# Performance work log

Hardware: AMD Instinct MI355X
Metric: run time of the kernel (lower is better)

Reference implementation:

```python
import jax, jax.numpy as jnp
import numpy as np

WINDOW_SIZE = 3
SIGMA = 1.5
C1 = 0.01 ** 2
C2 = 0.03 ** 2


def gaussian_window(channel, window_size=WINDOW_SIZE, sigma=SIGMA):
    x = jnp.arange(window_size, dtype=jnp.float32) - window_size // 2
    g1 = jnp.exp(-(x ** 2) / (2.0 * sigma ** 2))
    g1 = g1 / g1.sum()
    g2 = jnp.outer(g1, g1)  # [k, k]
    # depthwise kernel OIHW: [C, 1, k, k]
    return jnp.broadcast_to(g2, (channel, 1, window_size, window_size))


def depthwise_conv(x, window, channel, window_size=WINDOW_SIZE):
    pad = window_size // 2
    return jax.lax.conv_general_dilated(
        x, window,
        window_strides=(1, 1),
        padding=((pad, pad), (pad, pad)),
        dimension_numbers=('NCHW', 'OIHW', 'NCHW'),
        feature_group_count=channel,
    )


def setup_inputs() -> dict:
    key = jax.random.key(0)
    k1, k2 = jax.random.split(key)
    img1 = jax.random.uniform(k1, (32, 3, 512, 512), dtype=jnp.float32)
    img2 = jax.random.uniform(k2, (32, 3, 512, 512), dtype=jnp.float32)
    return {"img1": img1, "img2": img2}


def reference(img1, img2):
    channel = img1.shape[1]
    window = gaussian_window(channel)

    mu1 = depthwise_conv(img1, window, channel)
    mu2 = depthwise_conv(img2, window, channel)
    mu1_sq = mu1 * mu1
    mu2_sq = mu2 * mu2
    mu1_mu2 = mu1 * mu2

    sigma1_sq = depthwise_conv(img1 * img1, window, channel) - mu1_sq
    sigma2_sq = depthwise_conv(img2 * img2, window, channel) - mu2_sq
    sigma12 = depthwise_conv(img1 * img2, window, channel) - mu1_mu2

    ssim_map = ((2.0 * mu1_mu2 + C1) * (2.0 * sigma12 + C2)) / (
        (mu1_sq + mu2_sq + C1) * (sigma1_sq + sigma2_sq + C2))

    # size_sum defaults to True inside ssim() -> scalar sum
    return 1.0 - ssim_map.sum()
```

## Files before the change

kernel.cpp:

```cpp
#include <hip/hip_runtime.h>

#define IMG_H 512
#define IMG_W 512
#define RH 32


__global__ __launch_bounds__(256) void ssim_main_kernel(
    const float* __restrict__ img1, const float* __restrict__ img2,
    double* __restrict__ partial)
{
    constexpr float W_E = 0.30780133f;
    constexpr float W_C = 0.38439734f;
    constexpr float C1c = 1e-4f;
    constexpr float C2c = 9e-4f;

    const int t = threadIdx.x;
    const int y0 = blockIdx.x * RH;
    const size_t base = (size_t)blockIdx.y * (size_t)(IMG_H * IMG_W);
    const float* __restrict__ A = img1 + base;
    const float* __restrict__ B = img2 + base;
    const bool has_l = (t > 0);
    const bool has_r = (t < 255);
    const int x = 2 * t;

    float h1[2][3], h2[2][3], h11[2][3], h22[2][3], h12[2][3];

    float tsum = 0.0f;

    float a00, a01, a02, a03, b00, b01, b02, b03;
    float a10, a11, a12, a13, b10, b11, b12, b13;

#define LOADROW(AP, BP, OFF) do {                                   \
    const float2 _ma = *(const float2*)(A + (OFF));                 \
    const float2 _mb = *(const float2*)(B + (OFF));                 \
    AP##1 = _ma.x; AP##2 = _ma.y; BP##1 = _mb.x; BP##2 = _mb.y;     \
    AP##0 = has_l ? A[(OFF) - 1] : 0.0f;                            \
    AP##3 = has_r ? A[(OFF) + 2] : 0.0f;                            \
    BP##0 = has_l ? B[(OFF) - 1] : 0.0f;                            \
    BP##3 = has_r ? B[(OFF) + 2] : 0.0f;                            \
} while (0)

#define ZEROROW(AP, BP) do {                                        \
    AP##0 = 0.f; AP##1 = 0.f; AP##2 = 0.f; AP##3 = 0.f;             \
    BP##0 = 0.f; BP##1 = 0.f; BP##2 = 0.f; BP##3 = 0.f;             \
} while (0)

#define HPASS(AP, BP, S) do {                                               \
    const float sa0 = AP##0 * AP##0, sa1 = AP##1 * AP##1;                   \
    const float sa2 = AP##2 * AP##2, sa3 = AP##3 * AP##3;                   \
    const float sb0 = BP##0 * BP##0, sb1 = BP##1 * BP##1;                   \
    const float sb2 = BP##2 * BP##2, sb3 = BP##3 * BP##3;                   \
    const float p0 = AP##0 * BP##0, p1 = AP##1 * BP##1;                     \
    const float p2 = AP##2 * BP##2, p3 = AP##3 * BP##3;                     \
    h1[0][S]  = W_E * (AP##0 + AP##2) + W_C * AP##1;                        \
    h1[1][S]  = W_E * (AP##1 + AP##3) + W_C * AP##2;                        \
    h2[0][S]  = W_E * (BP##0 + BP##2) + W_C * BP##1;                        \
    h2[1][S]  = W_E * (BP##1 + BP##3) + W_C * BP##2;                        \
    h11[0][S] = W_E * (sa0 + sa2) + W_C * sa1;                              \
    h11[1][S] = W_E * (sa1 + sa3) + W_C * sa2;                              \
    h22[0][S] = W_E * (sb0 + sb2) + W_C * sb1;                              \
    h22[1][S] = W_E * (sb1 + sb3) + W_C * sb2;                              \
    h12[0][S] = W_E * (p0 + p2) + W_C * p1;                                 \
    h12[1][S] = W_E * (p1 + p3) + W_C * p2;                                 \
} while (0)

#define VOUT(E0, E1, MID) do {                                              \
    _Pragma("unroll")                                                       \
    for (int c = 0; c < 2; ++c) {                                           \
        const float mu1 = W_E * (h1[c][E0] + h1[c][E1]) + W_C * h1[c][MID]; \
        const float mu2 = W_E * (h2[c][E0] + h2[c][E1]) + W_C * h2[c][MID]; \
        const float e11 = W_E * (h11[c][E0] + h11[c][E1]) + W_C * h11[c][MID]; \
        const float e22 = W_E * (h22[c][E0] + h22[c][E1]) + W_C * h22[c][MID]; \
        const float e12 = W_E * (h12[c][E0] + h12[c][E1]) + W_C * h12[c][MID]; \
        const float mu1s = mu1 * mu1, mu2s = mu2 * mu2, m12 = mu1 * mu2;    \
        const float s11 = e11 - mu1s, s22 = e22 - mu2s, s12 = e12 - m12;    \
        const float num = (2.0f * m12 + C1c) * (2.0f * s12 + C2c);          \
        const float den = (mu1s + mu2s + C1c) * (s11 + s22 + C2c);          \
        tsum += num / den;                                                  \
    }                                                                       \
} while (0)

    size_t off = (size_t)y0 * IMG_W + x;

    if (blockIdx.x != 0) LOADROW(a0, b0, off - IMG_W); else ZEROROW(a0, b0);
    LOADROW(a1, b1, off);
    HPASS(a0, b0, 0);
    LOADROW(a0, b0, off + IMG_W);
    HPASS(a1, b1, 1);
    off += 2 * (size_t)IMG_W;

#pragma unroll 1
    for (int g = 0; g < 5; ++g) {
        LOADROW(a1, b1, off); off += IMG_W; HPASS(a0, b0, 2); VOUT(2, 0, 1);
        LOADROW(a0, b0, off); off += IMG_W; HPASS(a1, b1, 0); VOUT(0, 1, 2);
        LOADROW(a1, b1, off); off += IMG_W; HPASS(a0, b0, 1); VOUT(1, 2, 0);
        LOADROW(a0, b0, off); off += IMG_W; HPASS(a1, b1, 2); VOUT(2, 0, 1);
        LOADROW(a1, b1, off); off += IMG_W; HPASS(a0, b0, 0); VOUT(0, 1, 2);
        LOADROW(a0, b0, off); off += IMG_W; HPASS(a1, b1, 1); VOUT(1, 2, 0);
    }

    if (blockIdx.x != (IMG_H / RH - 1)) LOADROW(a1, b1, off); else ZEROROW(a1, b1);
    HPASS(a0, b0, 2); VOUT(2, 0, 1);
    HPASS(a1, b1, 0); VOUT(0, 1, 2);

#undef LOADROW
#undef ZEROROW
#undef HPASS
#undef VOUT

#pragma unroll
    for (int o = 32; o >= 1; o >>= 1)
        tsum += __shfl_xor(tsum, o, 64);

    __shared__ float wpart[4];
    if ((t & 63) == 0) wpart[t >> 6] = tsum;
    __syncthreads();
    if (t == 0) {
        partial[(size_t)blockIdx.y * gridDim.x + blockIdx.x] =
            (double)wpart[0] + (double)wpart[1] +
            (double)wpart[2] + (double)wpart[3];
    }
}

__global__ __launch_bounds__(256) void ssim_fin_kernel(
    const double* __restrict__ partial, float* __restrict__ out, int n)
{
    const int t = threadIdx.x;
    double s = 0.0;
    for (int i = t; i < n; i += 256) s += partial[i];
#pragma unroll
    for (int o = 32; o >= 1; o >>= 1)
        s += __shfl_xor(s, o, 64);
    __shared__ double w[4];
    if ((t & 63) == 0) w[t >> 6] = s;
    __syncthreads();
    if (t == 0)
        out[0] = 1.0f - (float)(w[0] + w[1] + w[2] + w[3]);
}

extern "C" void kernel_launch(void* const* d_in, const int* in_sizes, int n_in,
                              void* d_out, int out_size, void* d_ws, size_t ws_size,
                              hipStream_t stream) {
    const float* img1 = (const float*)d_in[0];
    const float* img2 = (const float*)d_in[1];
    float* out = (float*)d_out;
    double* partial = (double*)d_ws;

    const int planes = in_sizes[0] / (IMG_H * IMG_W);
    const int nblk = IMG_H / RH;

    dim3 grid(nblk, planes);
    ssim_main_kernel<<<grid, 256, 0, stream>>>(img1, img2, partial);
    ssim_fin_kernel<<<1, 256, 0, stream>>>(partial, out, nblk * planes);
}
```

Measured before the change: 227.7 us.

## Stage rows in double-buffered LDS and prefetch three rows ahead

```diff
diff --git a/kernel.cpp b/kernel.cpp
--- a/kernel.cpp
+++ b/kernel.cpp
@@ -3,7 +3,10 @@
 #define IMG_H 512
 #define IMG_W 512
 #define RH 32
+#define NBX (IMG_H / RH)
 
+
+typedef float v2f __attribute__((ext_vector_type(2), aligned(8)));
 
 __global__ __launch_bounds__(256) void ssim_main_kernel(
     const float* __restrict__ img1, const float* __restrict__ img2,
@@ -19,93 +22,127 @@
     const size_t base = (size_t)blockIdx.y * (size_t)(IMG_H * IMG_W);
     const float* __restrict__ A = img1 + base;
     const float* __restrict__ B = img2 + base;
-    const bool has_l = (t > 0);
-    const bool has_r = (t < 255);
     const int x = 2 * t;
 
+    __shared__ float lsA[2][3][520];
+    __shared__ float lsB[2][3][520];
+    if (t < 24) {
+        const int col = (t & 1) * 513;
+        const int q = t >> 1;
+        const int r = q % 3;
+        const int bu = (q / 3) & 1;
+        if (q < 6) lsA[bu][r][col] = 0.0f;
+        else       lsB[bu][r][col] = 0.0f;
+    }
+
+    v2f zz; zz.x = 0.0f; zz.y = 0.0f;
+
+    v2f sa0, sa1, sa2, sb0, sb1, sb2;
+
     float h1[2][3], h2[2][3], h11[2][3], h22[2][3], h12[2][3];
-
     float tsum = 0.0f;
 
-    float a00, a01, a02, a03, b00, b01, b02, b03;
-    float a10, a11, a12, a13, b10, b11, b12, b13;
-
-#define LOADROW(AP, BP, OFF) do {                                   \
-    const float2 _ma = *(const float2*)(A + (OFF));                 \
-    const float2 _mb = *(const float2*)(B + (OFF));                 \
-    AP##1 = _ma.x; AP##2 = _ma.y; BP##1 = _mb.x; BP##2 = _mb.y;     \
-    AP##0 = has_l ? A[(OFF) - 1] : 0.0f;                            \
-    AP##3 = has_r ? A[(OFF) + 2] : 0.0f;                            \
-    BP##0 = has_l ? B[(OFF) - 1] : 0.0f;                            \
-    BP##3 = has_r ? B[(OFF) + 2] : 0.0f;                            \
+#define LOAD3(SROW) do {                                                      \
+    const int g_ = (SROW);                                                    \
+    sa0 = (g_ >= 0 && g_ < IMG_H) ? *(const v2f*)(A + (size_t)g_ * IMG_W + x) : zz;       \
+    sb0 = (g_ >= 0 && g_ < IMG_H) ? *(const v2f*)(B + (size_t)g_ * IMG_W + x) : zz;       \
+    sa1 = (g_ + 1 < IMG_H) ? *(const v2f*)(A + (size_t)(g_ + 1) * IMG_W + x) : zz;        \
+    sb1 = (g_ + 1 < IMG_H) ? *(const v2f*)(B + (size_t)(g_ + 1) * IMG_W + x) : zz;        \
+    sa2 = (g_ + 2 < IMG_H) ? *(const v2f*)(A + (size_t)(g_ + 2) * IMG_W + x) : zz;        \
+    sb2 = (g_ + 2 < IMG_H) ? *(const v2f*)(B + (size_t)(g_ + 2) * IMG_W + x) : zz;        \
 } while (0)
 
-#define ZEROROW(AP, BP) do {                                        \
-    AP##0 = 0.f; AP##1 = 0.f; AP##2 = 0.f; AP##3 = 0.f;             \
-    BP##0 = 0.f; BP##1 = 0.f; BP##2 = 0.f; BP##3 = 0.f;             \
+#define WRITE3(BU) do {                                                       \
+    lsA[BU][0][1 + x] = sa0.x; lsA[BU][0][2 + x] = sa0.y;                     \
+    lsA[BU][1][1 + x] = sa1.x; lsA[BU][1][2 + x] = sa1.y;                     \
+    lsA[BU][2][1 + x] = sa2.x; lsA[BU][2][2 + x] = sa2.y;                     \
+    lsB[BU][0][1 + x] = sb0.x; lsB[BU][0][2 + x] = sb0.y;                     \
+    lsB[BU][1][1 + x] = sb1.x; lsB[BU][1][2 + x] = sb1.y;                     \
+    lsB[BU][2][1 + x] = sb2.x; lsB[BU][2][2 + x] = sb2.y;                     \
 } while (0)
 
-#define HPASS(AP, BP, S) do {                                               \
-    const float sa0 = AP##0 * AP##0, sa1 = AP##1 * AP##1;                   \
-    const float sa2 = AP##2 * AP##2, sa3 = AP##3 * AP##3;                   \
-    const float sb0 = BP##0 * BP##0, sb1 = BP##1 * BP##1;                   \
-    const float sb2 = BP##2 * BP##2, sb3 = BP##3 * BP##3;                   \
-    const float p0 = AP##0 * BP##0, p1 = AP##1 * BP##1;                     \
-    const float p2 = AP##2 * BP##2, p3 = AP##3 * BP##3;                     \
-    h1[0][S]  = W_E * (AP##0 + AP##2) + W_C * AP##1;                        \
-    h1[1][S]  = W_E * (AP##1 + AP##3) + W_C * AP##2;                        \
-    h2[0][S]  = W_E * (BP##0 + BP##2) + W_C * BP##1;                        \
-    h2[1][S]  = W_E * (BP##1 + BP##3) + W_C * BP##2;                        \
-    h11[0][S] = W_E * (sa0 + sa2) + W_C * sa1;                              \
-    h11[1][S] = W_E * (sa1 + sa3) + W_C * sa2;                              \
-    h22[0][S] = W_E * (sb0 + sb2) + W_C * sb1;                              \
-    h22[1][S] = W_E * (sb1 + sb3) + W_C * sb2;                              \
-    h12[0][S] = W_E * (p0 + p2) + W_C * p1;                                 \
-    h12[1][S] = W_E * (p1 + p3) + W_C * p2;                                 \
+#define HROW(BU, R, S) do {                                                   \
+    const v2f alo = *(const v2f*)&lsA[BU][R][x];                              \
+    const v2f ahi = *(const v2f*)&lsA[BU][R][x + 2];                          \
+    const v2f blo = *(const v2f*)&lsB[BU][R][x];                              \
+    const v2f bhi = *(const v2f*)&lsB[BU][R][x + 2];                          \
+    const float am = alo.x, a0 = alo.y, a1 = ahi.x, ap = ahi.y;               \
+    const float bm = blo.x, b0 = blo.y, b1 = bhi.x, bp = bhi.y;               \
+    const float qa0 = am * am, qa1 = a0 * a0, qa2 = a1 * a1, qa3 = ap * ap;   \
+    const float qb0 = bm * bm, qb1 = b0 * b0, qb2 = b1 * b1, qb3 = bp * bp;   \
+    const float p0 = am * bm, p1 = a0 * b0, p2 = a1 * b1, p3 = ap * bp;       \
+    h1[0][S]  = W_E * (am + a1) + W_C * a0;                                   \
+    h1[1][S]  = W_E * (a0 + ap) + W_C * a1;                                   \
+    h2[0][S]  = W_E * (bm + b1) + W_C * b0;                                   \
+    h2[1][S]  = W_E * (b0 + bp) + W_C * b1;                                   \
+    h11[0][S] = W_E * (qa0 + qa2) + W_C * qa1;                                \
+    h11[1][S] = W_E * (qa1 + qa3) + W_C * qa2;                                \
+    h22[0][S] = W_E * (qb0 + qb2) + W_C * qb1;                                \
+    h22[1][S] = W_E * (qb1 + qb3) + W_C * qb2;                                \
+    h12[0][S] = W_E * (p0 + p2) + W_C * p1;                                   \
+    h12[1][S] = W_E * (p1 + p3) + W_C * p2;                                   \
 } while (0)
 
-#define VOUT(E0, E1, MID) do {                                              \
-    _Pragma("unroll")                                                       \
-    for (int c = 0; c < 2; ++c) {                                           \
-        const float mu1 = W_E * (h1[c][E0] + h1[c][E1]) + W_C * h1[c][MID]; \
-        const float mu2 = W_E * (h2[c][E0] + h2[c][E1]) + W_C * h2[c][MID]; \
-        const float e11 = W_E * (h11[c][E0] + h11[c][E1]) + W_C * h11[c][MID]; \
-        const float e22 = W_E * (h22[c][E0] + h22[c][E1]) + W_C * h22[c][MID]; \
-        const float e12 = W_E * (h12[c][E0] + h12[c][E1]) + W_C * h12[c][MID]; \
-        const float mu1s = mu1 * mu1, mu2s = mu2 * mu2, m12 = mu1 * mu2;    \
-        const float s11 = e11 - mu1s, s22 = e22 - mu2s, s12 = e12 - m12;    \
-        const float num = (2.0f * m12 + C1c) * (2.0f * s12 + C2c);          \
-        const float den = (mu1s + mu2s + C1c) * (s11 + s22 + C2c);          \
-        tsum += num / den;                                                  \
-    }                                                                       \
+#define VOUT(E0, E1, MID) do {                                                \
+    _Pragma("unroll")                                                         \
+    for (int c = 0; c < 2; ++c) {                                             \
+        const float mu1 = W_E * (h1[c][E0] + h1[c][E1]) + W_C * h1[c][MID];   \
+        const float mu2 = W_E * (h2[c][E0] + h2[c][E1]) + W_C * h2[c][MID];   \
+        const float e11 = W_E * (h11[c][E0] + h11[c][E1]) + W_C * h11[c][MID];\
+        const float e22 = W_E * (h22[c][E0] + h22[c][E1]) + W_C * h22[c][MID];\
+        const float e12 = W_E * (h12[c][E0] + h12[c][E1]) + W_C * h12[c][MID];\
+        const float mu1s = mu1 * mu1, mu2s = mu2 * mu2, m12 = mu1 * mu2;      \
+        const float s11 = e11 - mu1s, s22 = e22 - mu2s, s12 = e12 - m12;      \
+        const float num = (2.0f * m12 + C1c) * (2.0f * s12 + C2c);            \
+        const float den = (mu1s + mu2s + C1c) * (s11 + s22 + C2c);            \
+        tsum += num / den;                                                    \
+    }                                                                         \
 } while (0)
 
-    size_t off = (size_t)y0 * IMG_W + x;
+    LOAD3(y0 - 1);
+    WRITE3(0);
+    LOAD3(y0 + 2);
+    __syncthreads();
 
-    if (blockIdx.x != 0) LOADROW(a0, b0, off - IMG_W); else ZEROROW(a0, b0);
-    LOADROW(a1, b1, off);
-    HPASS(a0, b0, 0);
-    LOADROW(a0, b0, off + IMG_W);
-    HPASS(a1, b1, 1);
-    off += 2 * (size_t)IMG_W;
+    WRITE3(1);
+    LOAD3(y0 + 5);
+    HROW(0, 0, 0);
+    HROW(0, 1, 1);
+    HROW(0, 2, 2); VOUT(2, 0, 1);
+    __syncthreads();
 
+    int srow = y0 + 8;
 #pragma unroll 1
-    for (int g = 0; g < 5; ++g) {
-        LOADROW(a1, b1, off); off += IMG_W; HPASS(a0, b0, 2); VOUT(2, 0, 1);
-        LOADROW(a0, b0, off); off += IMG_W; HPASS(a1, b1, 0); VOUT(0, 1, 2);
-        LOADROW(a1, b1, off); off += IMG_W; HPASS(a0, b0, 1); VOUT(1, 2, 0);
-        LOADROW(a0, b0, off); off += IMG_W; HPASS(a1, b1, 2); VOUT(2, 0, 1);
-        LOADROW(a1, b1, off); off += IMG_W; HPASS(a0, b0, 0); VOUT(0, 1, 2);
-        LOADROW(a0, b0, off); off += IMG_W; HPASS(a1, b1, 1); VOUT(1, 2, 0);
+    for (int p = 0; p < 4; ++p) {
+        WRITE3(0); LOAD3(srow); srow += 3;
+        HROW(1, 0, 0); VOUT(0, 1, 2);
+        HROW(1, 1, 1); VOUT(1, 2, 0);
+        HROW(1, 2, 2); VOUT(2, 0, 1);
+        __syncthreads();
+        WRITE3(1); LOAD3(srow); srow += 3;
+        HROW(0, 0, 0); VOUT(0, 1, 2);
+        HROW(0, 1, 1); VOUT(1, 2, 0);
+        HROW(0, 2, 2); VOUT(2, 0, 1);
+        __syncthreads();
     }
 
-    if (blockIdx.x != (IMG_H / RH - 1)) LOADROW(a1, b1, off); else ZEROROW(a1, b1);
-    HPASS(a0, b0, 2); VOUT(2, 0, 1);
-    HPASS(a1, b1, 0); VOUT(0, 1, 2);
+    WRITE3(0); LOAD3(srow);
+    HROW(1, 0, 0); VOUT(0, 1, 2);
+    HROW(1, 1, 1); VOUT(1, 2, 0);
+    HROW(1, 2, 2); VOUT(2, 0, 1);
+    __syncthreads();
 
-#undef LOADROW
-#undef ZEROROW
-#undef HPASS
+    WRITE3(1);
+    HROW(0, 0, 0); VOUT(0, 1, 2);
+    HROW(0, 1, 1); VOUT(1, 2, 0);
+    HROW(0, 2, 2); VOUT(2, 0, 1);
+    __syncthreads();
+
+    HROW(1, 0, 0); VOUT(0, 1, 2);
+
+#undef LOAD3
+#undef WRITE3
+#undef HROW
 #undef VOUT
 
 #pragma unroll
@@ -147,9 +184,8 @@
     double* partial = (double*)d_ws;
 
     const int planes = in_sizes[0] / (IMG_H * IMG_W);
-    const int nblk = IMG_H / RH;
 
-    dim3 grid(nblk, planes);
+    dim3 grid(NBX, planes);
     ssim_main_kernel<<<grid, 256, 0, stream>>>(img1, img2, partial);
-    ssim_fin_kernel<<<1, 256, 0, stream>>>(partial, out, nblk * planes);
+    ssim_fin_kernel<<<1, 256, 0, stream>>>(partial, out, NBX * planes);
 }
```

Result: no change. 225.8 us (-0.8%).
